# Performance work log

Measured on AMD Instinct MI355X. Metric: run time of the kernel, lower is better.

## Reference

```python
import jax, jax.numpy as jnp
import numpy as np

B, T, H = 65536, 24, 64  # batch, input_window_size, num_neurons
SLOPE = 25.0             # snntorch fast_sigmoid default slope

@jax.custom_vjp
def spike(x):
    # heaviside forward, fast-sigmoid surrogate backward
    return (x > 0).astype(x.dtype)

def _spike_fwd(x):
    return (x > 0).astype(x.dtype), x

def _spike_bwd(x, g):
    return (g / (SLOPE * jnp.abs(x) + 1.0) ** 2,)

spike.defvjp(_spike_fwd, _spike_bwd)

def slstm_cell(x, syn, mem, Wih, Whh, bih, bhh, thr):
    # snntorch SLSTM: LSTMCell with h=mem, c=syn; reset_mechanism='subtract'
    reset = jax.lax.stop_gradient((mem - thr > 0).astype(x.dtype))
    gates = x @ Wih.T + bih + mem @ Whh.T + bhh  # (B, 4H)
    i, f, g, o = jnp.split(gates, 4, axis=-1)
    syn_new = jax.nn.sigmoid(f) * syn + jax.nn.sigmoid(i) * jnp.tanh(g)
    mem_new = jax.nn.sigmoid(o) * jnp.tanh(syn_new) - reset * thr
    spk = spike(mem_new - thr)
    return spk, syn_new, mem_new

def setup_inputs() -> dict:
    key = jax.random.key(0)
    ks = jax.random.split(key, 11)
    s = float(1.0 / np.sqrt(H))  # LSTMCell uniform init bound
    so = float(1.0 / np.sqrt((T + 2) * H))
    u = lambda k, shape: jax.random.uniform(k, shape, jnp.float32, -s, s)
    return {
        "x": jax.random.normal(ks[0], (B, T, 1), jnp.float32),
        "Wih1": u(ks[1], (4 * H, 1)),
        "Whh1": u(ks[2], (4 * H, H)),
        "bih1": u(ks[3], (4 * H,)),
        "bhh1": u(ks[4], (4 * H,)),
        "thr1": jnp.float32(0.5),
        "Wih2": u(ks[5], (4 * H, H)),
        "Whh2": u(ks[6], (4 * H, H)),
        "bih2": u(ks[7], (4 * H,)),
        "bhh2": u(ks[8], (4 * H,)),
        "thr2": jnp.float32(0.5),
        "Wout": jax.random.uniform(ks[9], (2, (T + 2) * H), jnp.float32, -so, so),
        "bout": jnp.array([0.2, -0.2], jnp.float32),
    }

def reference(x, Wih1, Whh1, bih1, bhh1, thr1,
              Wih2, Whh2, bih2, bhh2, thr2, Wout, bout):
    Bn = x.shape[0]
    Hn = Whh1.shape[1]
    z = jnp.zeros((Bn, Hn), x.dtype)
    carry0 = (z, z, z, z)  # syn1, mem1, syn2, mem2

    def step(carry, xt):
        syn1, mem1, syn2, mem2 = carry
        spk1, syn1, mem1 = slstm_cell(xt, syn1, mem1, Wih1, Whh1, bih1, bhh1, thr1)
        spk2, syn2, mem2 = slstm_cell(spk1, syn2, mem2, Wih2, Whh2, bih2, bhh2, thr2)
        return (syn1, mem1, syn2, mem2), spk2

    (syn1, mem1, syn2, mem2), spk2_seq = jax.lax.scan(
        step, carry0, jnp.swapaxes(x, 0, 1))  # spk2_seq: (T, B, H)
    # extra step: feed mem1 into slstm2
    spk2_last, syn2, mem2 = slstm_cell(mem1, syn2, mem2, Wih2, Whh2, bih2, bhh2, thr2)
    lst = jnp.concatenate(
        [jnp.swapaxes(spk2_seq, 0, 1).reshape(Bn, -1), spk2_last, mem2], axis=1)
    return lst @ Wout.T + bout  # (B, 2)
```

## Files before the change

### kernel.cpp

```cpp
#include <hip/hip_runtime.h>
#include <cstdint>
#include <cstddef>


#define BB 65536
#define TT 24
#define NB 8

__device__ __forceinline__ float bcastf(float v, int l) {
  return __int_as_float(__builtin_amdgcn_readlane(__float_as_int(v), l));
}
__device__ __forceinline__ float sigm(float v) {
  return __fdividef(1.0f, 1.0f + __expf(-v));
}
__device__ __forceinline__ float tanh_fast(float v) {
  return fmaf(-2.0f, __fdividef(1.0f, __expf(2.0f * v) + 1.0f), 1.0f);
}
__device__ __forceinline__ float wsum(float v) {
#pragma unroll
  for (int o = 32; o > 0; o >>= 1) v += __shfl_xor(v, o);
  return v;
}

__global__ __attribute__((amdgpu_waves_per_eu(4, 4))) __launch_bounds__(512)
void snn_pass1(
    const float* __restrict__ x, const float* __restrict__ Wih1,
    const float* __restrict__ Whh1, const float* __restrict__ bih1,
    const float* __restrict__ bhh1, const float* __restrict__ thr1p,
    unsigned long long* __restrict__ spk_out, float* __restrict__ mem1_out) {
  __shared__ float4 P1[64][64];
  __shared__ float stM[8][64][NB];
  int tid = threadIdx.x;
  for (int idx = tid; idx < 16384; idx += 512) {
    int k = idx >> 6, m = idx & 63;
    ((float*)&P1[m][k & 63])[k >> 6] = Whh1[idx];
  }
  __syncthreads();
  int lane = tid & 63, wave = tid >> 6;
  int wb = (blockIdx.x * 8 + wave) * NB;
  float thr1 = thr1p[0];
  float b1q[4], wq[4];
#pragma unroll
  for (int q = 0; q < 4; q++) {
    b1q[q] = bih1[q * 64 + lane] + bhh1[q * 64 + lane];
    wq[q] = Wih1[q * 64 + lane];
  }
  float syn[NB], mem[NB];
#pragma unroll
  for (int b = 0; b < NB; b++) { syn[b] = 0.0f; mem[b] = 0.0f; }

  for (int t = 0; t < TT; t++) {
#pragma unroll
    for (int b = 0; b < NB; b++) stM[wave][lane][b] = mem[b];
    unsigned long long myspk = 0;
#pragma unroll
    for (int h = 0; h < 2; h++) {
      const int B0 = h * 4;
      float acc[4][4];
#pragma unroll
      for (int j = 0; j < 4; j++) {
        float xbt = x[(wb + B0 + j) * TT + t];
#pragma unroll
        for (int q = 0; q < 4; q++) acc[j][q] = fmaf(xbt, wq[q], b1q[q]);
      }
#pragma unroll 8
      for (int m = 0; m < 64; m++) {
        float4 w = P1[m][lane];
        float4 sa = *(const float4*)&stM[wave][m][B0];
        float s[4] = {sa.x, sa.y, sa.z, sa.w};
#pragma unroll
        for (int j = 0; j < 4; j++) {
          acc[j][0] = fmaf(s[j], w.x, acc[j][0]);
          acc[j][1] = fmaf(s[j], w.y, acc[j][1]);
          acc[j][2] = fmaf(s[j], w.z, acc[j][2]);
          acc[j][3] = fmaf(s[j], w.w, acc[j][3]);
        }
      }
#pragma unroll
      for (int j = 0; j < 4; j++) {
        int b = B0 + j;
        float ig = sigm(acc[j][0]), fg = sigm(acc[j][1]);
        float gg = tanh_fast(acc[j][2]), og = sigm(acc[j][3]);
        float sn = fmaf(fg, syn[b], ig * gg);
        float rst = (mem[b] > thr1) ? thr1 : 0.0f;
        float mn = fmaf(og, tanh_fast(sn), -rst);
        syn[b] = sn;
        mem[b] = mn;
        unsigned long long msk = __ballot(mn > thr1);
        if (lane == b) myspk = msk;
      }
      __builtin_amdgcn_sched_barrier(0);
    }
    if (lane < NB)
      spk_out[(size_t)t * BB + wb + lane] = myspk;
  }
#pragma unroll
  for (int b = 0; b < NB; b++)
    mem1_out[(size_t)(wb + b) * 64 + lane] = mem[b];
}

__global__ __attribute__((amdgpu_waves_per_eu(4, 4))) __launch_bounds__(1024)
void snn_pass2(
    const float* __restrict__ Wih2, const float* __restrict__ Whh2,
    const float* __restrict__ bih2, const float* __restrict__ bhh2,
    const float* __restrict__ thr2p, const float* __restrict__ Wout,
    const float* __restrict__ bout,
    const unsigned long long* __restrict__ spk_in,
    const float* __restrict__ mem1_in, float* __restrict__ out) {
  __shared__ float4 Pih[64][64];
  __shared__ float4 Phh[64][64];
  __shared__ float stM[16][64][NB];
  int tid = threadIdx.x;
  for (int idx = tid; idx < 16384; idx += 1024) {
    int k = idx >> 6, m = idx & 63;
    ((float*)&Pih[m][k & 63])[k >> 6] = Wih2[idx];
    ((float*)&Phh[m][k & 63])[k >> 6] = Whh2[idx];
  }
  __syncthreads();
  int lane = tid & 63, wave = tid >> 6;
  int wb = (blockIdx.x * 16 + wave) * NB;
  float thr2 = thr2p[0];
  float b2q[4];
#pragma unroll
  for (int q = 0; q < 4; q++) b2q[q] = bih2[q * 64 + lane] + bhh2[q * 64 + lane];
  float syn[NB], mem[NB];
  unsigned sb8[NB];
#pragma unroll
  for (int b = 0; b < NB; b++) { syn[b] = 0.0f; mem[b] = 0.0f; sb8[b] = 0u; }

  for (int t = 0; t < TT; t++) {
    unsigned long long mk[NB];
#pragma unroll
    for (int b = 0; b < NB; b++) {
      unsigned long long v = spk_in[(size_t)t * BB + wb + b];
      unsigned lo = __builtin_amdgcn_readfirstlane((unsigned)v);
      unsigned hi = __builtin_amdgcn_readfirstlane((unsigned)(v >> 32));
      mk[b] = ((unsigned long long)hi << 32) | (unsigned long long)lo;
    }
#pragma unroll
    for (int b = 0; b < NB; b++) stM[wave][lane][b] = mem[b];
#pragma unroll
    for (int h = 0; h < 2; h++) {
      const int B0 = h * 4;
      float acc[4][4];
#pragma unroll
      for (int j = 0; j < 4; j++) {
#pragma unroll
        for (int q = 0; q < 4; q++) acc[j][q] = b2q[q];
      }
#pragma unroll 4
      for (int m = 0; m < 64; m++) {
        float4 wh = Phh[m][lane];
        float4 sa = *(const float4*)&stM[wave][m][B0];
        float s[4] = {sa.x, sa.y, sa.z, sa.w};
#pragma unroll
        for (int j = 0; j < 4; j++) {
          acc[j][0] = fmaf(s[j], wh.x, acc[j][0]);
          acc[j][1] = fmaf(s[j], wh.y, acc[j][1]);
          acc[j][2] = fmaf(s[j], wh.z, acc[j][2]);
          acc[j][3] = fmaf(s[j], wh.w, acc[j][3]);
        }
      }
#pragma unroll
      for (int j = 0; j < 4; j++) {
        int b = B0 + j;
        unsigned long long k = mk[b];
        while (__builtin_popcountll(k) >= 4) {
          int m0 = __builtin_ctzll(k); k &= k - 1;
          int m1 = __builtin_ctzll(k); k &= k - 1;
          int m2 = __builtin_ctzll(k); k &= k - 1;
          int m3 = __builtin_ctzll(k); k &= k - 1;
          float4 r0 = Pih[m0][lane];
          float4 r1 = Pih[m1][lane];
          float4 r2 = Pih[m2][lane];
          float4 r3 = Pih[m3][lane];
          acc[j][0] += r0.x; acc[j][1] += r0.y; acc[j][2] += r0.z; acc[j][3] += r0.w;
          acc[j][0] += r1.x; acc[j][1] += r1.y; acc[j][2] += r1.z; acc[j][3] += r1.w;
          acc[j][0] += r2.x; acc[j][1] += r2.y; acc[j][2] += r2.z; acc[j][3] += r2.w;
          acc[j][0] += r3.x; acc[j][1] += r3.y; acc[j][2] += r3.z; acc[j][3] += r3.w;
        }
        while (k) {
          int m0 = __builtin_ctzll(k); k &= k - 1;
          float4 r0 = Pih[m0][lane];
          acc[j][0] += r0.x; acc[j][1] += r0.y; acc[j][2] += r0.z; acc[j][3] += r0.w;
        }
        float ig = sigm(acc[j][0]), fg = sigm(acc[j][1]);
        float gg = tanh_fast(acc[j][2]), og = sigm(acc[j][3]);
        float sn = fmaf(fg, syn[b], ig * gg);
        float rst = (mem[b] > thr2) ? thr2 : 0.0f;
        float mn = fmaf(og, tanh_fast(sn), -rst);
        syn[b] = sn;
        mem[b] = mn;
        sb8[b] |= (mn > thr2) ? (1u << t) : 0u;
      }
      __builtin_amdgcn_sched_barrier(0);
    }
  }

  float m1[NB];
#pragma unroll
  for (int b = 0; b < NB; b++) m1[b] = mem1_in[(size_t)(wb + b) * 64 + lane];
  float acc[NB][4];
#pragma unroll
  for (int b = 0; b < NB; b++) {
#pragma unroll
    for (int q = 0; q < 4; q++) acc[b][q] = b2q[q];
  }
#pragma unroll 4
  for (int m = 0; m < 64; m++) {
    float4 wi = Pih[m][lane];
    float4 wh = Phh[m][lane];
#pragma unroll
    for (int b = 0; b < NB; b++) {
      float s1 = bcastf(m1[b], m);
      float s2 = bcastf(mem[b], m);
      acc[b][0] = fmaf(s1, wi.x, fmaf(s2, wh.x, acc[b][0]));
      acc[b][1] = fmaf(s1, wi.y, fmaf(s2, wh.y, acc[b][1]));
      acc[b][2] = fmaf(s1, wi.z, fmaf(s2, wh.z, acc[b][2]));
      acc[b][3] = fmaf(s1, wi.w, fmaf(s2, wh.w, acc[b][3]));
    }
  }
  float p0[NB], p1[NB];
#pragma unroll
  for (int b = 0; b < NB; b++) { p0[b] = 0.0f; p1[b] = 0.0f; }
#pragma unroll 4
  for (int t = 0; t < TT; t++) {
    float w0 = Wout[t * 64 + lane];
    float w1 = Wout[1664 + t * 64 + lane];
#pragma unroll
    for (int b = 0; b < NB; b++) {
      float sf = ((sb8[b] >> t) & 1u) ? 1.0f : 0.0f;
      p0[b] = fmaf(sf, w0, p0[b]);
      p1[b] = fmaf(sf, w1, p1[b]);
    }
  }
  float wA0 = Wout[1536 + lane], wA1 = Wout[1664 + 1536 + lane];
  float wB0 = Wout[1600 + lane], wB1 = Wout[1664 + 1600 + lane];
  float bo0 = bout[0], bo1 = bout[1];
#pragma unroll
  for (int b = 0; b < NB; b++) {
    float ig = sigm(acc[b][0]), fg = sigm(acc[b][1]);
    float gg = tanh_fast(acc[b][2]), og = sigm(acc[b][3]);
    float sn = fmaf(fg, syn[b], ig * gg);
    float rst = (mem[b] > thr2) ? thr2 : 0.0f;
    float mn = fmaf(og, tanh_fast(sn), -rst);
    float sf = (mn > thr2) ? 1.0f : 0.0f;
    p0[b] = fmaf(sf, wA0, p0[b]);
    p1[b] = fmaf(sf, wA1, p1[b]);
    p0[b] = fmaf(mn, wB0, p0[b]);
    p1[b] = fmaf(mn, wB1, p1[b]);
  }
  float vout = 0.0f;
#pragma unroll
  for (int b = 0; b < NB; b++) {
    float r0 = wsum(p0[b]);
    float r1 = wsum(p1[b]);
    if (lane == 2 * b) vout = r0;
    if (lane == 2 * b + 1) vout = r1;
  }
  if (lane < 2 * NB)
    out[(size_t)wb * 2 + lane] = vout + ((lane & 1) ? bo1 : bo0);
}

extern "C" void kernel_launch(void* const* d_in, const int* in_sizes, int n_in,
                              void* d_out, int out_size, void* d_ws, size_t ws_size,
                              hipStream_t stream) {
  const float* x = (const float*)d_in[0];
  const float* Wih1 = (const float*)d_in[1];
  const float* Whh1 = (const float*)d_in[2];
  const float* bih1 = (const float*)d_in[3];
  const float* bhh1 = (const float*)d_in[4];
  const float* thr1 = (const float*)d_in[5];
  const float* Wih2 = (const float*)d_in[6];
  const float* Whh2 = (const float*)d_in[7];
  const float* bih2 = (const float*)d_in[8];
  const float* bhh2 = (const float*)d_in[9];
  const float* thr2 = (const float*)d_in[10];
  const float* Wout = (const float*)d_in[11];
  const float* bout = (const float*)d_in[12];

  unsigned long long* spk = (unsigned long long*)d_ws;
  float* mem1 = (float*)((char*)d_ws + (size_t)TT * BB * 8);

  snn_pass1<<<BB / (8 * NB), 512, 0, stream>>>(x, Wih1, Whh1, bih1, bhh1, thr1,
                                               spk, mem1);
  snn_pass2<<<BB / (16 * NB), 1024, 0, stream>>>(Wih2, Whh2, bih2, bhh2, thr2,
                                                 Wout, bout, spk, mem1,
                                                 (float*)d_out);
}
```

Baseline: 1.784 ms.

## Fuse both SLSTM layers into one kernel, reading layer-1 weights from global

Merges the two passes into one kernel so layer-1 spike masks and final mem1 stay in registers. This removes the global spike buffer write/read and the mem1 round trip. Layer-1 recurrent weights are prepacked by a small kernel and read from global/L2 each step instead of LDS, since LDS now holds the layer-2 matrices. x is preloaded per lane and broadcast with readlane. The risks are higher register pressure and L2/global load latency in the layer-1 inner loop.

```diff
diff --git a/kernel.cpp b/kernel.cpp
--- a/kernel.cpp
+++ b/kernel.cpp
@@ -22,50 +22,77 @@
   return v;
 }
 
-__global__ __attribute__((amdgpu_waves_per_eu(4, 4))) __launch_bounds__(512)
-void snn_pass1(
+__global__ __launch_bounds__(1024) void prepack_p1t(
+    const float* __restrict__ Whh1, float4* __restrict__ p1t) {
+  int i = blockIdx.x * 1024 + threadIdx.x;
+  if (i < 4096) {
+    int m = i >> 6, l = i & 63;
+    p1t[i] = make_float4(Whh1[l * 64 + m], Whh1[(64 + l) * 64 + m],
+                         Whh1[(128 + l) * 64 + m], Whh1[(192 + l) * 64 + m]);
+  }
+}
+
+__global__ __attribute__((amdgpu_waves_per_eu(4, 4))) __launch_bounds__(1024)
+void snn_fused(
     const float* __restrict__ x, const float* __restrict__ Wih1,
-    const float* __restrict__ Whh1, const float* __restrict__ bih1,
+    const float4* __restrict__ P1T, const float* __restrict__ bih1,
     const float* __restrict__ bhh1, const float* __restrict__ thr1p,
-    unsigned long long* __restrict__ spk_out, float* __restrict__ mem1_out) {
-  __shared__ float4 P1[64][64];
-  __shared__ float stM[8][64][NB];
+    const float* __restrict__ Wih2, const float* __restrict__ Whh2,
+    const float* __restrict__ bih2, const float* __restrict__ bhh2,
+    const float* __restrict__ thr2p, const float* __restrict__ Wout,
+    const float* __restrict__ bout, float* __restrict__ out) {
+  __shared__ float4 Pih[64][64];
+  __shared__ float4 Phh[64][64];
+  __shared__ float stM[16][64][NB];
   int tid = threadIdx.x;
-  for (int idx = tid; idx < 16384; idx += 512) {
+  int lane = tid & 63, wave = tid >> 6;
+  int wb = (blockIdx.x * 16 + wave) * NB;
+
+  float xv[NB];
+  int lt = (lane < TT) ? lane : (TT - 1);
+#pragma unroll
+  for (int b = 0; b < NB; b++) xv[b] = x[(size_t)(wb + b) * TT + lt];
+
+  for (int idx = tid; idx < 16384; idx += 1024) {
     int k = idx >> 6, m = idx & 63;
-    ((float*)&P1[m][k & 63])[k >> 6] = Whh1[idx];
+    ((float*)&Pih[m][k & 63])[k >> 6] = Wih2[idx];
+    ((float*)&Phh[m][k & 63])[k >> 6] = Whh2[idx];
   }
   __syncthreads();
-  int lane = tid & 63, wave = tid >> 6;
-  int wb = (blockIdx.x * 8 + wave) * NB;
-  float thr1 = thr1p[0];
-  float b1q[4], wq[4];
+
+  float thr1 = thr1p[0], thr2 = thr2p[0];
+  float b1q[4], wq[4], b2q[4];
 #pragma unroll
   for (int q = 0; q < 4; q++) {
     b1q[q] = bih1[q * 64 + lane] + bhh1[q * 64 + lane];
     wq[q] = Wih1[q * 64 + lane];
-  }
-  float syn[NB], mem[NB];
-#pragma unroll
-  for (int b = 0; b < NB; b++) { syn[b] = 0.0f; mem[b] = 0.0f; }
+    b2q[q] = bih2[q * 64 + lane] + bhh2[q * 64 + lane];
+  }
+  float syn1[NB], mem1[NB], syn2[NB], mem2[NB];
+  unsigned sb8[NB];
+#pragma unroll
+  for (int b = 0; b < NB; b++) {
+    syn1[b] = 0.0f; mem1[b] = 0.0f; syn2[b] = 0.0f; mem2[b] = 0.0f;
+    sb8[b] = 0u;
+  }
+  unsigned long long mk[NB];
 
   for (int t = 0; t < TT; t++) {
 #pragma unroll
-    for (int b = 0; b < NB; b++) stM[wave][lane][b] = mem[b];
-    unsigned long long myspk = 0;
+    for (int b = 0; b < NB; b++) stM[wave][lane][b] = mem1[b];
 #pragma unroll
     for (int h = 0; h < 2; h++) {
       const int B0 = h * 4;
       float acc[4][4];
 #pragma unroll
       for (int j = 0; j < 4; j++) {
-        float xbt = x[(wb + B0 + j) * TT + t];
+        float xbt = bcastf(xv[B0 + j], t);
 #pragma unroll
         for (int q = 0; q < 4; q++) acc[j][q] = fmaf(xbt, wq[q], b1q[q]);
       }
 #pragma unroll 8
       for (int m = 0; m < 64; m++) {
-        float4 w = P1[m][lane];
+        float4 w = P1T[m * 64 + lane];
         float4 sa = *(const float4*)&stM[wave][m][B0];
         float s[4] = {sa.x, sa.y, sa.z, sa.w};
 #pragma unroll
@@ -81,64 +108,17 @@
         int b = B0 + j;
         float ig = sigm(acc[j][0]), fg = sigm(acc[j][1]);
         float gg = tanh_fast(acc[j][2]), og = sigm(acc[j][3]);
-        float sn = fmaf(fg, syn[b], ig * gg);
-        float rst = (mem[b] > thr1) ? thr1 : 0.0f;
+        float sn = fmaf(fg, syn1[b], ig * gg);
+        float rst = (mem1[b] > thr1) ? thr1 : 0.0f;
         float mn = fmaf(og, tanh_fast(sn), -rst);
-        syn[b] = sn;
-        mem[b] = mn;
-        unsigned long long msk = __ballot(mn > thr1);
-        if (lane == b) myspk = msk;
+        syn1[b] = sn;
+        mem1[b] = mn;
+        mk[b] = __ballot(mn > thr1);
       }
       __builtin_amdgcn_sched_barrier(0);
     }
-    if (lane < NB)
-      spk_out[(size_t)t * BB + wb + lane] = myspk;
-  }
-#pragma unroll
-  for (int b = 0; b < NB; b++)
-    mem1_out[(size_t)(wb + b) * 64 + lane] = mem[b];
-}
-
-__global__ __attribute__((amdgpu_waves_per_eu(4, 4))) __launch_bounds__(1024)
-void snn_pass2(
-    const float* __restrict__ Wih2, const float* __restrict__ Whh2,
-    const float* __restrict__ bih2, const float* __restrict__ bhh2,
-    const float* __restrict__ thr2p, const float* __restrict__ Wout,
-    const float* __restrict__ bout,
-    const unsigned long long* __restrict__ spk_in,
-    const float* __restrict__ mem1_in, float* __restrict__ out) {
-  __shared__ float4 Pih[64][64];
-  __shared__ float4 Phh[64][64];
-  __shared__ float stM[16][64][NB];
-  int tid = threadIdx.x;
-  for (int idx = tid; idx < 16384; idx += 1024) {
-    int k = idx >> 6, m = idx & 63;
-    ((float*)&Pih[m][k & 63])[k >> 6] = Wih2[idx];
-    ((float*)&Phh[m][k & 63])[k >> 6] = Whh2[idx];
-  }
-  __syncthreads();
-  int lane = tid & 63, wave = tid >> 6;
-  int wb = (blockIdx.x * 16 + wave) * NB;
-  float thr2 = thr2p[0];
-  float b2q[4];
-#pragma unroll
-  for (int q = 0; q < 4; q++) b2q[q] = bih2[q * 64 + lane] + bhh2[q * 64 + lane];
-  float syn[NB], mem[NB];
-  unsigned sb8[NB];
-#pragma unroll
-  for (int b = 0; b < NB; b++) { syn[b] = 0.0f; mem[b] = 0.0f; sb8[b] = 0u; }
-
-  for (int t = 0; t < TT; t++) {
-    unsigned long long mk[NB];
-#pragma unroll
-    for (int b = 0; b < NB; b++) {
-      unsigned long long v = spk_in[(size_t)t * BB + wb + b];
-      unsigned lo = __builtin_amdgcn_readfirstlane((unsigned)v);
-      unsigned hi = __builtin_amdgcn_readfirstlane((unsigned)(v >> 32));
-      mk[b] = ((unsigned long long)hi << 32) | (unsigned long long)lo;
-    }
-#pragma unroll
-    for (int b = 0; b < NB; b++) stM[wave][lane][b] = mem[b];
+#pragma unroll
+    for (int b = 0; b < NB; b++) stM[wave][lane][b] = mem2[b];
 #pragma unroll
     for (int h = 0; h < 2; h++) {
       const int B0 = h * 4;
@@ -186,20 +166,17 @@
         }
         float ig = sigm(acc[j][0]), fg = sigm(acc[j][1]);
         float gg = tanh_fast(acc[j][2]), og = sigm(acc[j][3]);
-        float sn = fmaf(fg, syn[b], ig * gg);
-        float rst = (mem[b] > thr2) ? thr2 : 0.0f;
+        float sn = fmaf(fg, syn2[b], ig * gg);
+        float rst = (mem2[b] > thr2) ? thr2 : 0.0f;
         float mn = fmaf(og, tanh_fast(sn), -rst);
-        syn[b] = sn;
-        mem[b] = mn;
+        syn2[b] = sn;
+        mem2[b] = mn;
         sb8[b] |= (mn > thr2) ? (1u << t) : 0u;
       }
       __builtin_amdgcn_sched_barrier(0);
     }
   }
 
-  float m1[NB];
-#pragma unroll
-  for (int b = 0; b < NB; b++) m1[b] = mem1_in[(size_t)(wb + b) * 64 + lane];
   float acc[NB][4];
 #pragma unroll
   for (int b = 0; b < NB; b++) {
@@ -212,8 +189,8 @@
     float4 wh = Phh[m][lane];
 #pragma unroll
     for (int b = 0; b < NB; b++) {
-      float s1 = bcastf(m1[b], m);
-      float s2 = bcastf(mem[b], m);
+      float s1 = bcastf(mem1[b], m);
+      float s2 = bcastf(mem2[b], m);
       acc[b][0] = fmaf(s1, wi.x, fmaf(s2, wh.x, acc[b][0]));
       acc[b][1] = fmaf(s1, wi.y, fmaf(s2, wh.y, acc[b][1]));
       acc[b][2] = fmaf(s1, wi.z, fmaf(s2, wh.z, acc[b][2]));
@@ -241,8 +218,8 @@
   for (int b = 0; b < NB; b++) {
     float ig = sigm(acc[b][0]), fg = sigm(acc[b][1]);
     float gg = tanh_fast(acc[b][2]), og = sigm(acc[b][3]);
-    float sn = fmaf(fg, syn[b], ig * gg);
-    float rst = (mem[b] > thr2) ? thr2 : 0.0f;
+    float sn = fmaf(fg, syn2[b], ig * gg);
+    float rst = (mem2[b] > thr2) ? thr2 : 0.0f;
     float mn = fmaf(og, tanh_fast(sn), -rst);
     float sf = (mn > thr2) ? 1.0f : 0.0f;
     p0[b] = fmaf(sf, wA0, p0[b]);
@@ -279,12 +256,10 @@
   const float* Wout = (const float*)d_in[11];
   const float* bout = (const float*)d_in[12];
 
-  unsigned long long* spk = (unsigned long long*)d_ws;
-  float* mem1 = (float*)((char*)d_ws + (size_t)TT * BB * 8);
-
-  snn_pass1<<<BB / (8 * NB), 512, 0, stream>>>(x, Wih1, Whh1, bih1, bhh1, thr1,
-                                               spk, mem1);
-  snn_pass2<<<BB / (16 * NB), 1024, 0, stream>>>(Wih2, Whh2, bih2, bhh2, thr2,
-                                                 Wout, bout, spk, mem1,
-                                                 (float*)d_out);
-}
+  float4* p1t = (float4*)d_ws;
+
+  prepack_p1t<<<4, 1024, 0, stream>>>(Whh1, p1t);
+  snn_fused<<<BB / (16 * NB), 1024, 0, stream>>>(
+      x, Wih1, p1t, bih1, bhh1, thr1, Wih2, Whh2, bih2, bhh2, thr2, Wout, bout,
+      (float*)d_out);
+}
```

Measured after the change: 2.051 ms. 14.9% more time.
